# Kernel tuning notes

Hardware: AMD Instinct MI355X
Metric: run time of the kernel (lower is better)

## Reference

```python
import jax, jax.numpy as jnp
import numpy as np

ALPHA = 0.2          # LeakyReLU negative slope (Alpha)
NEG_INF = -9e15      # mask value used by pygat-style GAT


def _masked_attention(Wh, a_src, a_dst, mask):
    """Wh: [H,N,d], a_src/a_dst: [H,d], mask: [N,N] (nonzero = edge).
    Returns attention-aggregated features [H,N,d]."""
    f_src = jnp.einsum('hnd,hd->hn', Wh, a_src)   # [H,N]
    f_dst = jnp.einsum('hnd,hd->hn', Wh, a_dst)   # [H,N]
    e = jax.nn.leaky_relu(f_src[:, :, None] + f_dst[:, None, :], ALPHA)  # [H,N,N]
    e = jnp.where(mask[None, :, :] > 0, e, NEG_INF)
    att = jax.nn.softmax(e, axis=-1)              # masked softmax over neighbors
    return jnp.einsum('hnm,hmd->hnd', att, Wh)    # [H,N,d]


def setup_inputs() -> dict:
    key = jax.random.key(0)
    ks = jax.random.split(key, 8)
    N, F_in, D, H = 4096, 512, 64, 8
    x = jax.random.normal(ks[0], (N, F_in), dtype=jnp.float32)
    adj = jax.random.randint(ks[1], (N, N), 0, 2, dtype=jnp.int32)
    s = 0.1
    W = jax.random.normal(ks[2], (H, F_in, D), dtype=jnp.float32) * s
    a_src = jax.random.normal(ks[3], (H, D), dtype=jnp.float32) * s
    a_dst = jax.random.normal(ks[4], (H, D), dtype=jnp.float32) * s
    W_o = jax.random.normal(ks[5], (H * D, D), dtype=jnp.float32) * s
    ao_src = jax.random.normal(ks[6], (D,), dtype=jnp.float32) * s
    ao_dst = jax.random.normal(ks[7], (D,), dtype=jnp.float32) * s
    return {"x": x, "adj": adj, "W": W, "a_src": a_src, "a_dst": a_dst,
            "W_o": W_o, "ao_src": ao_src, "ao_dst": ao_dst}


def reference(x, adj, W, a_src, a_dst, W_o, ao_src, ao_dst):
    N = x.shape[0]
    # --- multi-head layer (concat=True: ELU per head, concat on feature dim) ---
    Wh = jnp.einsum('nf,hfd->hnd', x, W)                     # [H,N,d]
    h1 = jax.nn.elu(_masked_attention(Wh, a_src, a_dst, adj))  # [H,N,d]
    h_cat = jnp.transpose(h1, (1, 0, 2)).reshape(N, -1)      # [N, H*d]
    # --- output head (concat=False: no ELU inside layer) ---
    Who = (h_cat @ W_o)[None]                                # [1,N,d]
    h2 = _masked_attention(Who, ao_src[None], ao_dst[None], adj)[0]  # [N,d]
    # GAT.forward: activation (ELU) then log_softmax over dim=1
    return jax.nn.log_softmax(jax.nn.elu(h2), axis=1)
```

## Files before the change

### kernel.cpp

```cpp
#include <hip/hip_runtime.h>
#include <hip/hip_bf16.h>
#include <math.h>

#define N_NODES 4096
#define FDIM 512
#define D 64
#define H 8
#define NWORDS (N_NODES / 64)

typedef __attribute__((ext_vector_type(8))) short bf16x8;
typedef __attribute__((ext_vector_type(4))) float f32x4;

__device__ inline short f2bf(float x) {
    return (short)((__builtin_bit_cast(unsigned int, x) + 0x8000u) >> 16);
}
__device__ inline float b2f(unsigned short s) {
    return __builtin_bit_cast(float, (unsigned int)s << 16);
}

__device__ inline int sext_bit(unsigned int v, int j) {
#if defined(__has_builtin) && __has_builtin(__builtin_amdgcn_sbfe)
    return __builtin_amdgcn_sbfe((int)v, j, 1);
#else
    return ((int)(v << (31 - j))) >> 31;
#endif
}

__device__ inline unsigned fenc(float f) {
    unsigned u = __builtin_bit_cast(unsigned, f);
    return (u & 0x80000000u) ? ~u : (u | 0x80000000u);
}
__device__ inline float fdec(unsigned e) {
    unsigned u = (e & 0x80000000u) ? (e & 0x7FFFFFFFu) : ~e;
    return __builtin_bit_cast(float, u);
}

__device__ inline void gl2lds16(const void* g, void* l) {
#if defined(__has_builtin) && __has_builtin(__builtin_amdgcn_global_load_lds)
    __builtin_amdgcn_global_load_lds(
        (const __attribute__((address_space(1))) unsigned int*)g,
        (__attribute__((address_space(3))) unsigned int*)l, 16, 0, 0);
#else
    *(uint4*)l = *(const uint4*)g;
#endif
}

#define NB_BITS (N_NODES * N_NODES / 2048)
#define NB_X    (N_NODES * FDIM / 1024)
#define NB_W    (H * FDIM * D / 256)
#define NB_WO   (FDIM * D / 256)
__global__ void k_pre(const int* __restrict__ adj, const float* __restrict__ x,
                      const float* __restrict__ W, const float* __restrict__ Wo,
                      unsigned int* __restrict__ bits32, short* __restrict__ Xbf,
                      short* __restrict__ WF, short* __restrict__ WoF,
                      float* __restrict__ cm1, float* __restrict__ cm2,
                      unsigned* __restrict__ gmaxe1, unsigned* __restrict__ gmaxe2) {
    const int b = blockIdx.x, t = threadIdx.x;
    if (b == 0) {
        for (int i = t; i < H * D; i += 256) cm1[i] = 0.f;
        if (t < D) cm2[t] = 0.f;
        if (t < H) gmaxe1[t] = 0u;
        if (t == 0) gmaxe2[0] = 0u;
        return;
    }
    if (b < 1 + NB_BITS) {
        const int tid  = (b - 1) * 256 + t;
        const size_t e0 = (size_t)tid * 8;
        int4 a0 = *(const int4*)&adj[e0];
        int4 a1 = *(const int4*)&adj[e0 + 4];
        unsigned by = (unsigned)(a0.x != 0)       | ((unsigned)(a0.y != 0) << 1)
                    | ((unsigned)(a0.z != 0) << 2) | ((unsigned)(a0.w != 0) << 3)
                    | ((unsigned)(a1.x != 0) << 4) | ((unsigned)(a1.y != 0) << 5)
                    | ((unsigned)(a1.z != 0) << 6) | ((unsigned)(a1.w != 0) << 7);
        unsigned v = by | (__shfl_xor((int)by, 1) << 8);
        v = v | ((unsigned)__shfl_xor((int)v, 2) << 16);
        if ((t & 3) == 0) bits32[tid >> 2] = v;
        return;
    }
    if (b < 1 + NB_BITS + NB_X) {
        const size_t i4 = ((size_t)(b - 1 - NB_BITS) * 256 + t) * 4;
        float4 v = *(const float4*)&x[i4];
        ushort4 o;
        o.x = (unsigned short)f2bf(v.x); o.y = (unsigned short)f2bf(v.y);
        o.z = (unsigned short)f2bf(v.z); o.w = (unsigned short)f2bf(v.w);
        *(ushort4*)&Xbf[i4] = o;
        return;
    }
    if (b < 1 + NB_BITS + NB_X + NB_W) {
        const size_t idx = (size_t)(b - 1 - NB_BITS - NB_X) * 256 + t;
        const int d = idx & 63;
        const int k = (int)(idx >> 6) & 511;
        const int h = (int)(idx >> 15);
        WF[(((size_t)h * 64 + (k >> 3)) * 64 + d) * 8 + (k & 7)] = f2bf(W[idx]);
        return;
    }
    {
        const size_t idx = (size_t)(b - 1 - NB_BITS - NB_X - NB_W) * 256 + t;
        const int d = idx & 63;
        const int k = (int)(idx >> 6);
        WoF[(((size_t)(k >> 3)) * 64 + d) * 8 + (k & 7)] = f2bf(Wo[idx]);
    }
}

__global__ void __launch_bounds__(256) k_gemm(
    const short* __restrict__ Xbf, const short* __restrict__ WF,
    const float* __restrict__ av, const float* __restrict__ bv,
    short* __restrict__ WBout, float* __restrict__ fs, float* __restrict__ fd,
    unsigned* __restrict__ gmaxe, float* __restrict__ cm) {
    const int h  = blockIdx.y;
    const int i0 = blockIdx.x * 64;
    const int t = threadIdx.x, w = t >> 6, lane = t & 63;
    const int li = lane & 15, quad = lane >> 4, k0 = quad * 8;
    const int row_a = i0 + w * 16 + li;
    const short* __restrict__ Xr  = Xbf + (size_t)row_a * FDIM;
    const short* __restrict__ WFh = WF + (size_t)h * 64 * D * 8;

    f32x4 c0 = {0.f, 0.f, 0.f, 0.f}, c1 = c0, c2 = c0, c3 = c0;
    #pragma unroll 4
    for (int kt = 0; kt < FDIM; kt += 32) {
        bf16x8 a = *(const bf16x8*)&Xr[kt + k0];
        const short* bb = WFh + (size_t)((kt >> 3) + quad) * (D * 8) + li * 8;
        bf16x8 b0 = *(const bf16x8*)(bb);
        bf16x8 b1 = *(const bf16x8*)(bb + 128);
        bf16x8 b2 = *(const bf16x8*)(bb + 256);
        bf16x8 b3 = *(const bf16x8*)(bb + 384);
        c0 = __builtin_amdgcn_mfma_f32_16x16x32_bf16(a, b0, c0, 0, 0, 0);
        c1 = __builtin_amdgcn_mfma_f32_16x16x32_bf16(a, b1, c1, 0, 0, 0);
        c2 = __builtin_amdgcn_mfma_f32_16x16x32_bf16(a, b2, c2, 0, 0, 0);
        c3 = __builtin_amdgcn_mfma_f32_16x16x32_bf16(a, b3, c3, 0, 0, 0);
    }
    float av4[4], bv4[4];
    #pragma unroll
    for (int t4 = 0; t4 < 4; ++t4) {
        av4[t4] = av[h * D + t4 * 16 + li];
        bv4[t4] = bv[h * D + t4 * 16 + li];
    }
    float tiles[4][4];
    #pragma unroll
    for (int r = 0; r < 4; ++r) { tiles[0][r] = c0[r]; tiles[1][r] = c1[r]; tiles[2][r] = c2[r]; tiles[3][r] = c3[r]; }

    __shared__ float csum[4][64];
    __shared__ float red[4];
    float fdmax = -INFINITY;
    float s4[4] = {0.f, 0.f, 0.f, 0.f};

    #pragma unroll
    for (int r = 0; r < 4; ++r) {
        const int row = i0 + w * 16 + quad * 4 + r;
        float pa = 0.f, pb = 0.f;
        #pragma unroll
        for (int t4 = 0; t4 < 4; ++t4) {
            const float v = tiles[t4][r];
            const int d = t4 * 16 + li;
            WBout[((size_t)h * (N_NODES / 8) + (row >> 3)) * (D * 8) + d * 8 + (row & 7)] = f2bf(v);
            pa += v * av4[t4];
            pb += v * bv4[t4];
            s4[t4] += v;
        }
        #pragma unroll
        for (int off = 1; off < 16; off <<= 1) {
            pa += __shfl_xor(pa, off);
            pb += __shfl_xor(pb, off);
        }
        if (li == 0) {
            fs[(size_t)h * N_NODES + row] = pa;
            fd[(size_t)h * N_NODES + row] = pb;
        }
        fdmax = fmaxf(fdmax, pb);
    }
    fdmax = fmaxf(fdmax, __shfl_xor(fdmax, 16));
    fdmax = fmaxf(fdmax, __shfl_xor(fdmax, 32));
    if (lane == 0) red[w] = fdmax;
    #pragma unroll
    for (int t4 = 0; t4 < 4; ++t4) {
        s4[t4] += __shfl_xor(s4[t4], 16);
        s4[t4] += __shfl_xor(s4[t4], 32);
    }
    if (quad == 0)
        #pragma unroll
        for (int t4 = 0; t4 < 4; ++t4) csum[w][t4 * 16 + li] = s4[t4];
    __syncthreads();
    if (t == 0)
        atomicMax(gmaxe + h, fenc(fmaxf(fmaxf(red[0], red[1]), fmaxf(red[2], red[3]))));
    if (t < 64)
        atomicAdd(&cm[h * D + t],
                  (csum[0][t] + csum[1][t] + csum[2][t] + csum[3][t]) * (1.f / (float)N_NODES));
}

__global__ void __launch_bounds__(256, 3) k_accum(
    const unsigned int* __restrict__ bits32,
    const short* __restrict__ WB,
    const float* __restrict__ fsb, const float* __restrict__ fdb,
    const unsigned* __restrict__ gmaxe,
    short* __restrict__ num, float* __restrict__ den, int kslab) {

    __shared__ __align__(16) short Bt[2][16 * 64 * 8];
    __shared__ __align__(16) float Esh[512];
    __shared__ __align__(16) float Gsh[512];

    const int h = blockIdx.y, i0 = blockIdx.x * 256, slab = blockIdx.z;
    const int t = threadIdx.x, w = t >> 6, lane = t & 63;
    const int li = lane & 15, quad = lane >> 4, k0 = quad * 8;
    const size_t ho = (size_t)h * N_NODES;
    const float  gm = fdec(gmaxe[h]);
    const float* __restrict__ fd = fdb + ho;
    const short* __restrict__ Bh = WB + (size_t)h * (N_NODES / 8) * D * 8;

    const int k_beg = slab * kslab;
    const int ntile = kslab / 128;

    auto stage = [&](int buf, int jtile) {
        const short* src = Bh + (size_t)(jtile >> 3) * (D * 8);
        #pragma unroll
        for (int p = 0; p < 4; ++p)
            gl2lds16(src + (size_t)(p * 256 + t) * 8, &Bt[buf][(p * 256 + t) * 8]);
    };

    int bito[4];
    #pragma unroll
    for (int f = 0; f < 4; ++f)
        bito[f] = (i0 + w * 64 + f * 16 + li) * (NWORDS * 2);
    uint4 bw[4];
    #pragma unroll
    for (int f = 0; f < 4; ++f)
        bw[f] = *(const uint4*)&bits32[(size_t)bito[f] + (k_beg >> 5)];
    stage(0, k_beg);
    {
        const int jj = t * 2;
        if (jj < kslab) {
            float2 f2 = *(const float2*)&fd[k_beg + jj];
            Esh[jj]     = __expf(f2.x - gm);
            Esh[jj + 1] = __expf(f2.y - gm);
            Gsh[jj]     = __expf(0.2f * (f2.x - gm));
            Gsh[jj + 1] = __expf(0.2f * (f2.y - gm));
        }
    }
    float Rv[4];
    #pragma unroll
    for (int f = 0; f < 4; ++f)
        Rv[f] = __expf(-0.8f * (fsb[ho + i0 + w * 64 + f * 16 + li] + gm));

    f32x4 acc[4][4], c5[4];
    #pragma unroll
    for (int f = 0; f < 4; ++f) {
        #pragma unroll
        for (int q = 0; q < 4; ++q) acc[f][q] = (f32x4){0.f, 0.f, 0.f, 0.f};
        c5[f] = (f32x4){0.f, 0.f, 0.f, 0.f};
    }
    bf16x8 ones;
    #pragma unroll
    for (int j = 0; j < 8; ++j) ones[j] = (short)0x3F80;

    __syncthreads();

    for (int tile = 0; tile < ntile; ++tile) {
        const int jt = k_beg + tile * 128;
        __builtin_amdgcn_s_barrier();
        if (tile > 0) {
            #pragma unroll
            for (int f = 0; f < 4; ++f)
                bw[f] = *(const uint4*)&bits32[(size_t)bito[f] + (jt >> 5)];
        }
        if (tile + 1 < ntile) {
            stage((tile + 1) & 1, jt + 128);
            asm volatile("s_waitcnt vmcnt(4)" ::: "memory");
        } else {
            asm volatile("s_waitcnt vmcnt(0)" ::: "memory");
        }
        __builtin_amdgcn_s_barrier();

        const short* Bl = Bt[tile & 1];
        const float* Ee = Esh + tile * 128;
        const float* Gg = Gsh + tile * 128;
        #pragma unroll
        for (int s = 0; s < 4; ++s) {
            const float4 e0 = *(const float4*)&Ee[s * 32 + k0];
            const float4 e1 = *(const float4*)&Ee[s * 32 + k0 + 4];
            const float4 g0 = *(const float4*)&Gg[s * 32 + k0];
            const float4 g1 = *(const float4*)&Gg[s * 32 + k0 + 4];
            float ev[8], gv[8];
            ev[0] = e0.x; ev[1] = e0.y; ev[2] = e0.z; ev[3] = e0.w;
            ev[4] = e1.x; ev[5] = e1.y; ev[6] = e1.z; ev[7] = e1.w;
            gv[0] = g0.x; gv[1] = g0.y; gv[2] = g0.z; gv[3] = g0.w;
            gv[4] = g1.x; gv[5] = g1.y; gv[6] = g1.z; gv[7] = g1.w;
            const short* bb = Bl + (size_t)((s * 4 + quad) * 64 + li) * 8;
            bf16x8 b0 = *(const bf16x8*)(bb);
            bf16x8 b1 = *(const bf16x8*)(bb + 128);
            bf16x8 b2 = *(const bf16x8*)(bb + 256);
            bf16x8 b3 = *(const bf16x8*)(bb + 384);
            #pragma unroll
            for (int f = 0; f < 4; ++f) {
                const unsigned int wsel = (s == 0) ? bw[f].x : (s == 1) ? bw[f].y
                                        : (s == 2) ? bw[f].z : bw[f].w;
                const unsigned int byt = (wsel >> k0) & 0xFFu;
                unsigned int pa[8];
                #pragma unroll
                for (int j = 0; j < 8; ++j) {
                    const float p = fmaxf(ev[j], gv[j] * Rv[f]);
                    pa[j] = __builtin_bit_cast(unsigned int, p)
                            & (unsigned int)sext_bit(byt, j);
                }
                bf16x8 a;
                unsigned int* au = (unsigned int*)&a;
                au[0] = __builtin_amdgcn_perm(pa[1], pa[0], 0x07060302);
                au[1] = __builtin_amdgcn_perm(pa[3], pa[2], 0x07060302);
                au[2] = __builtin_amdgcn_perm(pa[5], pa[4], 0x07060302);
                au[3] = __builtin_amdgcn_perm(pa[7], pa[6], 0x07060302);
                __builtin_amdgcn_s_setprio(1);
                acc[f][0] = __builtin_amdgcn_mfma_f32_16x16x32_bf16(a, b0, acc[f][0], 0, 0, 0);
                acc[f][1] = __builtin_amdgcn_mfma_f32_16x16x32_bf16(a, b1, acc[f][1], 0, 0, 0);
                acc[f][2] = __builtin_amdgcn_mfma_f32_16x16x32_bf16(a, b2, acc[f][2], 0, 0, 0);
                acc[f][3] = __builtin_amdgcn_mfma_f32_16x16x32_bf16(a, b3, acc[f][3], 0, 0, 0);
                c5[f]     = __builtin_amdgcn_mfma_f32_16x16x32_bf16(a, ones, c5[f], 0, 0, 0);
                __builtin_amdgcn_s_setprio(0);
            }
        }
    }

    const size_t so = (size_t)(slab * gridDim.y + h);
    #pragma unroll
    for (int f = 0; f < 4; ++f) {
        #pragma unroll
        for (int t4 = 0; t4 < 4; ++t4)
            #pragma unroll
            for (int r = 0; r < 4; ++r) {
                const int row = i0 + w * 64 + f * 16 + quad * 4 + r;
                num[(so * N_NODES + row) * D + t4 * 16 + li] = f2bf(acc[f][t4][r]);
            }
        if (li == 0)
            #pragma unroll
            for (int r = 0; r < 4; ++r)
                den[so * N_NODES + i0 + w * 64 + f * 16 + quad * 4 + r] = c5[f][r];
    }
}

__global__ void k_post1(const short* __restrict__ num, const float* __restrict__ den,
                        const float* __restrict__ colmean, short* __restrict__ hcat) {
    const int h   = blockIdx.y;
    const int i0  = blockIdx.x * 64;
    const int t   = threadIdx.x;
    const int row = i0 + (t >> 2);
    const int cb  = (t & 3) * 16;
    const size_t HN = (size_t)gridDim.y * N_NODES;
    const size_t r0 = (size_t)h * N_NODES + row;
    float dsum = 0.f;
    #pragma unroll
    for (int s = 0; s < 8; ++s) dsum += den[s * HN + r0];
    const bool  uni  = !(dsum > 0.f);
    const float linv = uni ? 0.f : 1.f / dsum;
    #pragma unroll
    for (int c = 0; c < 4; ++c) {
        const int col = cb + c * 4;
        float4 v = {0.f, 0.f, 0.f, 0.f};
        #pragma unroll
        for (int s = 0; s < 8; ++s) {
            ushort4 a = *(const ushort4*)&num[(s * HN + r0) * D + col];
            v.x += b2f(a.x); v.y += b2f(a.y); v.z += b2f(a.z); v.w += b2f(a.w);
        }
        v.x *= linv; v.y *= linv; v.z *= linv; v.w *= linv;
        if (uni) v = *(const float4*)&colmean[h * D + col];
        v.x = v.x > 0.f ? v.x : __expf(v.x) - 1.f;
        v.y = v.y > 0.f ? v.y : __expf(v.y) - 1.f;
        v.z = v.z > 0.f ? v.z : __expf(v.z) - 1.f;
        v.w = v.w > 0.f ? v.w : __expf(v.w) - 1.f;
        ushort4 o;
        o.x = (unsigned short)f2bf(v.x); o.y = (unsigned short)f2bf(v.y);
        o.z = (unsigned short)f2bf(v.z); o.w = (unsigned short)f2bf(v.w);
        *(ushort4*)&hcat[(size_t)row * (H * D) + h * D + col] = o;
    }
}

__global__ void k_lsm(const short* __restrict__ num, const float* __restrict__ den,
                      const float* __restrict__ cm, float* __restrict__ out) {
    const int n    = blockIdx.x * 4 + (threadIdx.x >> 6);
    const int lane = threadIdx.x & 63;
    float v = 0.f, ds = 0.f;
    #pragma unroll
    for (int s = 0; s < 32; ++s)
        v += b2f((unsigned short)num[((size_t)s * N_NODES + n) * D + lane]);
    #pragma unroll
    for (int s = 0; s < 32; ++s) ds += den[(size_t)s * N_NODES + n];
    v = (ds > 0.f) ? v / ds : cm[lane];
    v = v > 0.f ? v : __expf(v) - 1.f;
    float mx = v;
    #pragma unroll
    for (int off = 32; off > 0; off >>= 1) mx = fmaxf(mx, __shfl_xor(mx, off));
    float ex = __expf(v - mx);
    float sum = ex;
    #pragma unroll
    for (int off = 32; off > 0; off >>= 1) sum += __shfl_xor(sum, off);
    out[(size_t)n * D + lane] = (v - mx) - __logf(sum);
}

extern "C" void kernel_launch(void* const* d_in, const int* in_sizes, int n_in,
                              void* d_out, int out_size, void* d_ws, size_t ws_size,
                              hipStream_t stream) {
    const float* x      = (const float*)d_in[0];
    const int*   adj    = (const int*)d_in[1];
    const float* W      = (const float*)d_in[2];
    const float* a_src  = (const float*)d_in[3];
    const float* a_dst  = (const float*)d_in[4];
    const float* W_o    = (const float*)d_in[5];
    const float* ao_src = (const float*)d_in[6];
    const float* ao_dst = (const float*)d_in[7];
    float* out = (float*)d_out;

    char* wsp = (char*)d_ws;
    size_t off = 0;
    auto alloc = [&](size_t bytes) -> void* {
        void* p = wsp + off;
        off += (bytes + 255) & ~(size_t)255;
        return p;
    };
    unsigned* adj_bits = (unsigned*)alloc((size_t)N_NODES * NWORDS * 8);
    short*    Xbf   = (short*)alloc((size_t)N_NODES * FDIM * 2);
    short*    WF1   = (short*)alloc((size_t)H * 64 * D * 8 * 2);
    short*    WoF   = (short*)alloc((size_t)64 * D * 8 * 2);
    short*    WhB   = (short*)alloc((size_t)H * N_NODES * D * 2);
    float*    fs1   = (float*)alloc((size_t)H * N_NODES * 4);
    float*    fd1   = (float*)alloc((size_t)H * N_NODES * 4);
    unsigned* gme1  = (unsigned*)alloc((size_t)H * 4);
    float*    cm1   = (float*)alloc((size_t)H * D * 4);
    short*    num1  = (short*)alloc((size_t)8 * H * N_NODES * D * 2);
    float*    den1  = (float*)alloc((size_t)8 * H * N_NODES * 4);
    short*    hcat  = (short*)alloc((size_t)N_NODES * H * D * 2);
    short*    WhoB  = (short*)alloc((size_t)N_NODES * D * 2);
    float*    fs2   = (float*)alloc((size_t)N_NODES * 4);
    float*    fd2   = (float*)alloc((size_t)N_NODES * 4);
    unsigned* gme2  = (unsigned*)alloc(4);
    float*    cm2   = (float*)alloc((size_t)D * 4);
    short*    num2  = (short*)alloc((size_t)32 * N_NODES * D * 2);
    float*    den2  = (float*)alloc((size_t)32 * N_NODES * 4);

    k_pre  <<<dim3(1 + NB_BITS + NB_X + NB_W + NB_WO), dim3(256), 0, stream>>>(
        adj, x, W, W_o, adj_bits, Xbf, WF1, WoF, cm1, cm2, gme1, gme2);

    k_gemm <<<dim3(N_NODES / 64, H), dim3(256), 0, stream>>>(Xbf, WF1, a_src, a_dst,
                                                             WhB, fs1, fd1, gme1, cm1);
    k_accum<<<dim3(N_NODES / 256, H, 8), dim3(256), 0, stream>>>(adj_bits, WhB, fs1, fd1, gme1,
                                                                 num1, den1, N_NODES / 8);
    k_post1<<<dim3(N_NODES / 64, H), dim3(256), 0, stream>>>(num1, den1, cm1, hcat);

    k_gemm <<<dim3(N_NODES / 64, 1), dim3(256), 0, stream>>>(hcat, WoF, ao_src, ao_dst,
                                                             WhoB, fs2, fd2, gme2, cm2);
    k_accum<<<dim3(N_NODES / 256, 1, 32), dim3(256), 0, stream>>>(adj_bits, WhoB, fs2, fd2, gme2,
                                                                  num2, den2, N_NODES / 32);
    k_lsm  <<<dim3(N_NODES / 4), dim3(256), 0, stream>>>(num2, den2, cm2, out);
}
```

Baseline: 203.5 us.

## Switch bf16 pipeline to fp16 with packed half-precision attention weight computation

Converts all intermediate storage and MFMA operations from bf16 to fp16, and computes the masked attention probabilities in k_accum using packed f16x2 multiply/max instead of per-element fp32 math followed by truncating perms. Esh/Gsh shared arrays shrink to half-precision, halving LDS footprint and reads in the inner loop. This reduces VALU work in the hot accumulation loop, but fp16's narrower range risks overflow or underflow of exp values, activations and accumulated partial sums stored as fp16.

Result: no change. 201.1 us (-1.2%).

```diff
diff --git a/kernel.cpp b/kernel.cpp
--- a/kernel.cpp
+++ b/kernel.cpp
@@ -10,13 +10,18 @@
 
 typedef __attribute__((ext_vector_type(8))) short bf16x8;
 typedef __attribute__((ext_vector_type(4))) float f32x4;
-
-__device__ inline short f2bf(float x) {
-    return (short)((__builtin_bit_cast(unsigned int, x) + 0x8000u) >> 16);
-}
-__device__ inline float b2f(unsigned short s) {
-    return __builtin_bit_cast(float, (unsigned int)s << 16);
-}
+typedef __attribute__((ext_vector_type(8))) _Float16 f16x8;
+typedef __attribute__((ext_vector_type(2))) _Float16 f16x2;
+typedef __attribute__((ext_vector_type(4))) unsigned int u32x4;
+
+__device__ inline short f2h(float x) {
+    _Float16 h = (_Float16)x;
+    return __builtin_bit_cast(short, h);
+}
+__device__ inline float h2f(unsigned short u) {
+    return (float)__builtin_bit_cast(_Float16, u);
+}
+__device__ inline f16x2 bcH(unsigned int u) { return __builtin_bit_cast(f16x2, u); }
 
 __device__ inline int sext_bit(unsigned int v, int j) {
 #if defined(__has_builtin) && __has_builtin(__builtin_amdgcn_sbfe)
@@ -81,8 +86,8 @@
         const size_t i4 = ((size_t)(b - 1 - NB_BITS) * 256 + t) * 4;
         float4 v = *(const float4*)&x[i4];
         ushort4 o;
-        o.x = (unsigned short)f2bf(v.x); o.y = (unsigned short)f2bf(v.y);
-        o.z = (unsigned short)f2bf(v.z); o.w = (unsigned short)f2bf(v.w);
+        o.x = (unsigned short)f2h(v.x); o.y = (unsigned short)f2h(v.y);
+        o.z = (unsigned short)f2h(v.z); o.w = (unsigned short)f2h(v.w);
         *(ushort4*)&Xbf[i4] = o;
         return;
     }
@@ -91,14 +96,14 @@
         const int d = idx & 63;
         const int k = (int)(idx >> 6) & 511;
         const int h = (int)(idx >> 15);
-        WF[(((size_t)h * 64 + (k >> 3)) * 64 + d) * 8 + (k & 7)] = f2bf(W[idx]);
+        WF[(((size_t)h * 64 + (k >> 3)) * 64 + d) * 8 + (k & 7)] = f2h(W[idx]);
         return;
     }
     {
         const size_t idx = (size_t)(b - 1 - NB_BITS - NB_X - NB_W) * 256 + t;
         const int d = idx & 63;
         const int k = (int)(idx >> 6);
-        WoF[(((size_t)(k >> 3)) * 64 + d) * 8 + (k & 7)] = f2bf(Wo[idx]);
+        WoF[(((size_t)(k >> 3)) * 64 + d) * 8 + (k & 7)] = f2h(Wo[idx]);
     }
 }
 
@@ -118,16 +123,16 @@
     f32x4 c0 = {0.f, 0.f, 0.f, 0.f}, c1 = c0, c2 = c0, c3 = c0;
     #pragma unroll 4
     for (int kt = 0; kt < FDIM; kt += 32) {
-        bf16x8 a = *(const bf16x8*)&Xr[kt + k0];
+        f16x8 a = __builtin_bit_cast(f16x8, *(const bf16x8*)&Xr[kt + k0]);
         const short* bb = WFh + (size_t)((kt >> 3) + quad) * (D * 8) + li * 8;
-        bf16x8 b0 = *(const bf16x8*)(bb);
-        bf16x8 b1 = *(const bf16x8*)(bb + 128);
-        bf16x8 b2 = *(const bf16x8*)(bb + 256);
-        bf16x8 b3 = *(const bf16x8*)(bb + 384);
-        c0 = __builtin_amdgcn_mfma_f32_16x16x32_bf16(a, b0, c0, 0, 0, 0);
-        c1 = __builtin_amdgcn_mfma_f32_16x16x32_bf16(a, b1, c1, 0, 0, 0);
-        c2 = __builtin_amdgcn_mfma_f32_16x16x32_bf16(a, b2, c2, 0, 0, 0);
-        c3 = __builtin_amdgcn_mfma_f32_16x16x32_bf16(a, b3, c3, 0, 0, 0);
+        f16x8 b0 = __builtin_bit_cast(f16x8, *(const bf16x8*)(bb));
+        f16x8 b1 = __builtin_bit_cast(f16x8, *(const bf16x8*)(bb + 128));
+        f16x8 b2 = __builtin_bit_cast(f16x8, *(const bf16x8*)(bb + 256));
+        f16x8 b3 = __builtin_bit_cast(f16x8, *(const bf16x8*)(bb + 384));
+        c0 = __builtin_amdgcn_mfma_f32_16x16x32_f16(a, b0, c0, 0, 0, 0);
+        c1 = __builtin_amdgcn_mfma_f32_16x16x32_f16(a, b1, c1, 0, 0, 0);
+        c2 = __builtin_amdgcn_mfma_f32_16x16x32_f16(a, b2, c2, 0, 0, 0);
+        c3 = __builtin_amdgcn_mfma_f32_16x16x32_f16(a, b3, c3, 0, 0, 0);
     }
     float av4[4], bv4[4];
     #pragma unroll
@@ -152,7 +157,7 @@
         for (int t4 = 0; t4 < 4; ++t4) {
             const float v = tiles[t4][r];
             const int d = t4 * 16 + li;
-            WBout[((size_t)h * (N_NODES / 8) + (row >> 3)) * (D * 8) + d * 8 + (row & 7)] = f2bf(v);
+            WBout[((size_t)h * (N_NODES / 8) + (row >> 3)) * (D * 8) + d * 8 + (row & 7)] = f2h(v);
             pa += v * av4[t4];
             pb += v * bv4[t4];
             s4[t4] += v;
@@ -195,8 +200,8 @@
     short* __restrict__ num, float* __restrict__ den, int kslab) {
 
     __shared__ __align__(16) short Bt[2][16 * 64 * 8];
-    __shared__ __align__(16) float Esh[512];
-    __shared__ __align__(16) float Gsh[512];
+    __shared__ __align__(16) short Esh[512];
+    __shared__ __align__(16) short Gsh[512];
 
     const int h = blockIdx.y, i0 = blockIdx.x * 256, slab = blockIdx.z;
     const int t = threadIdx.x, w = t >> 6, lane = t & 63;
@@ -229,16 +234,20 @@
         const int jj = t * 2;
         if (jj < kslab) {
             float2 f2 = *(const float2*)&fd[k_beg + jj];
-            Esh[jj]     = __expf(f2.x - gm);
-            Esh[jj + 1] = __expf(f2.y - gm);
-            Gsh[jj]     = __expf(0.2f * (f2.x - gm));
-            Gsh[jj + 1] = __expf(0.2f * (f2.y - gm));
-        }
-    }
-    float Rv[4];
-    #pragma unroll
-    for (int f = 0; f < 4; ++f)
-        Rv[f] = __expf(-0.8f * (fsb[ho + i0 + w * 64 + f * 16 + li] + gm));
+            f16x2 ep = {(_Float16)__expf(f2.x - gm), (_Float16)__expf(f2.y - gm)};
+            f16x2 gp = {(_Float16)__expf(0.2f * (f2.x - gm)),
+                        (_Float16)__expf(0.2f * (f2.y - gm))};
+            *(f16x2*)&Esh[jj] = ep;
+            *(f16x2*)&Gsh[jj] = gp;
+        }
+    }
+    f16x2 Rp[4];
+    #pragma unroll
+    for (int f = 0; f < 4; ++f) {
+        const float rv = __expf(-0.8f * (fsb[ho + i0 + w * 64 + f * 16 + li] + gm));
+        const _Float16 rh = (_Float16)rv;
+        Rp[f] = (f16x2){rh, rh};
+    }
 
     f32x4 acc[4][4], c5[4];
     #pragma unroll
@@ -247,9 +256,10 @@
         for (int q = 0; q < 4; ++q) acc[f][q] = (f32x4){0.f, 0.f, 0.f, 0.f};
         c5[f] = (f32x4){0.f, 0.f, 0.f, 0.f};
     }
-    bf16x8 ones;
-    #pragma unroll
-    for (int j = 0; j < 8; ++j) ones[j] = (short)0x3F80;
+    bf16x8 ones_;
+    #pragma unroll
+    for (int j = 0; j < 8; ++j) ones_[j] = (short)0x3C00;
+    const f16x8 ones = __builtin_bit_cast(f16x8, ones_);
 
     __syncthreads();
 
@@ -270,48 +280,41 @@
         __builtin_amdgcn_s_barrier();
 
         const short* Bl = Bt[tile & 1];
-        const float* Ee = Esh + tile * 128;
-        const float* Gg = Gsh + tile * 128;
+        const short* Ee = Esh + tile * 128;
+        const short* Gg = Gsh + tile * 128;
         #pragma unroll
         for (int s = 0; s < 4; ++s) {
-            const float4 e0 = *(const float4*)&Ee[s * 32 + k0];
-            const float4 e1 = *(const float4*)&Ee[s * 32 + k0 + 4];
-            const float4 g0 = *(const float4*)&Gg[s * 32 + k0];
-            const float4 g1 = *(const float4*)&Gg[s * 32 + k0 + 4];
-            float ev[8], gv[8];
-            ev[0] = e0.x; ev[1] = e0.y; ev[2] = e0.z; ev[3] = e0.w;
-            ev[4] = e1.x; ev[5] = e1.y; ev[6] = e1.z; ev[7] = e1.w;
-            gv[0] = g0.x; gv[1] = g0.y; gv[2] = g0.z; gv[3] = g0.w;
-            gv[4] = g1.x; gv[5] = g1.y; gv[6] = g1.z; gv[7] = g1.w;
+            const uint4 Eu = *(const uint4*)&Ee[s * 32 + k0];
+            const uint4 Gu = *(const uint4*)&Gg[s * 32 + k0];
+            f16x2 Ep[4] = {bcH(Eu.x), bcH(Eu.y), bcH(Eu.z), bcH(Eu.w)};
+            f16x2 Gp[4] = {bcH(Gu.x), bcH(Gu.y), bcH(Gu.z), bcH(Gu.w)};
             const short* bb = Bl + (size_t)((s * 4 + quad) * 64 + li) * 8;
-            bf16x8 b0 = *(const bf16x8*)(bb);
-            bf16x8 b1 = *(const bf16x8*)(bb + 128);
-            bf16x8 b2 = *(const bf16x8*)(bb + 256);
-            bf16x8 b3 = *(const bf16x8*)(bb + 384);
+            f16x8 b0 = __builtin_bit_cast(f16x8, *(const bf16x8*)(bb));
+            f16x8 b1 = __builtin_bit_cast(f16x8, *(const bf16x8*)(bb + 128));
+            f16x8 b2 = __builtin_bit_cast(f16x8, *(const bf16x8*)(bb + 256));
+            f16x8 b3 = __builtin_bit_cast(f16x8, *(const bf16x8*)(bb + 384));
             #pragma unroll
             for (int f = 0; f < 4; ++f) {
                 const unsigned int wsel = (s == 0) ? bw[f].x : (s == 1) ? bw[f].y
                                         : (s == 2) ? bw[f].z : bw[f].w;
                 const unsigned int byt = (wsel >> k0) & 0xFFu;
-                unsigned int pa[8];
+                u32x4 au;
                 #pragma unroll
-                for (int j = 0; j < 8; ++j) {
-                    const float p = fmaxf(ev[j], gv[j] * Rv[f]);
-                    pa[j] = __builtin_bit_cast(unsigned int, p)
-                            & (unsigned int)sext_bit(byt, j);
+                for (int d2 = 0; d2 < 4; ++d2) {
+                    const unsigned mw = (unsigned)__builtin_amdgcn_perm(
+                        (unsigned)sext_bit(byt, 2 * d2 + 1),
+                        (unsigned)sext_bit(byt, 2 * d2), 0x05040100u);
+                    const f16x2 tv = Gp[d2] * Rp[f];
+                    const f16x2 pv = __builtin_elementwise_max(Ep[d2], tv);
+                    au[d2] = __builtin_bit_cast(unsigned, pv) & mw;
                 }
-                bf16x8 a;
-                unsigned int* au = (unsigned int*)&a;
-                au[0] = __builtin_amdgcn_perm(pa[1], pa[0], 0x07060302);
-                au[1] = __builtin_amdgcn_perm(pa[3], pa[2], 0x07060302);
-                au[2] = __builtin_amdgcn_perm(pa[5], pa[4], 0x07060302);
-                au[3] = __builtin_amdgcn_perm(pa[7], pa[6], 0x07060302);
+                const f16x8 a = __builtin_bit_cast(f16x8, au);
                 __builtin_amdgcn_s_setprio(1);
-                acc[f][0] = __builtin_amdgcn_mfma_f32_16x16x32_bf16(a, b0, acc[f][0], 0, 0, 0);
-                acc[f][1] = __builtin_amdgcn_mfma_f32_16x16x32_bf16(a, b1, acc[f][1], 0, 0, 0);
-                acc[f][2] = __builtin_amdgcn_mfma_f32_16x16x32_bf16(a, b2, acc[f][2], 0, 0, 0);
-                acc[f][3] = __builtin_amdgcn_mfma_f32_16x16x32_bf16(a, b3, acc[f][3], 0, 0, 0);
-                c5[f]     = __builtin_amdgcn_mfma_f32_16x16x32_bf16(a, ones, c5[f], 0, 0, 0);
+                acc[f][0] = __builtin_amdgcn_mfma_f32_16x16x32_f16(a, b0, acc[f][0], 0, 0, 0);
+                acc[f][1] = __builtin_amdgcn_mfma_f32_16x16x32_f16(a, b1, acc[f][1], 0, 0, 0);
+                acc[f][2] = __builtin_amdgcn_mfma_f32_16x16x32_f16(a, b2, acc[f][2], 0, 0, 0);
+                acc[f][3] = __builtin_amdgcn_mfma_f32_16x16x32_f16(a, b3, acc[f][3], 0, 0, 0);
+                c5[f]     = __builtin_amdgcn_mfma_f32_16x16x32_f16(a, ones, c5[f], 0, 0, 0);
                 __builtin_amdgcn_s_setprio(0);
             }
         }
@@ -325,7 +328,7 @@
             #pragma unroll
             for (int r = 0; r < 4; ++r) {
                 const int row = i0 + w * 64 + f * 16 + quad * 4 + r;
-                num[(so * N_NODES + row) * D + t4 * 16 + li] = f2bf(acc[f][t4][r]);
+                num[(so * N_NODES + row) * D + t4 * 16 + li] = f2h(acc[f][t4][r]);
             }
         if (li == 0)
             #pragma unroll
@@ -355,7 +358,7 @@
         #pragma unroll
         for (int s = 0; s < 8; ++s) {
             ushort4 a = *(const ushort4*)&num[(s * HN + r0) * D + col];
-            v.x += b2f(a.x); v.y += b2f(a.y); v.z += b2f(a.z); v.w += b2f(a.w);
+            v.x += h2f(a.x); v.y += h2f(a.y); v.z += h2f(a.z); v.w += h2f(a.w);
         }
         v.x *= linv; v.y *= linv; v.z *= linv; v.w *= linv;
         if (uni) v = *(const float4*)&colmean[h * D + col];
@@ -364,8 +367,8 @@
         v.z = v.z > 0.f ? v.z : __expf(v.z) - 1.f;
         v.w = v.w > 0.f ? v.w : __expf(v.w) - 1.f;
         ushort4 o;
-        o.x = (unsigned short)f2bf(v.x); o.y = (unsigned short)f2bf(v.y);
-        o.z = (unsigned short)f2bf(v.z); o.w = (unsigned short)f2bf(v.w);
+        o.x = (unsigned short)f2h(v.x); o.y = (unsigned short)f2h(v.y);
+        o.z = (unsigned short)f2h(v.z); o.w = (unsigned short)f2h(v.w);
         *(ushort4*)&hcat[(size_t)row * (H * D) + h * D + col] = o;
     }
 }
@@ -377,7 +380,7 @@
     float v = 0.f, ds = 0.f;
     #pragma unroll
     for (int s = 0; s < 32; ++s)
-        v += b2f((unsigned short)num[((size_t)s * N_NODES + n) * D + lane]);
+        v += h2f((unsigned short)num[((size_t)s * N_NODES + n) * D + lane]);
     #pragma unroll
     for (int s = 0; s < 32; ++s) ds += den[(size_t)s * N_NODES + n];
     v = (ds > 0.f) ? v / ds : cm[lane];
```
